# Optimization experiments

Measured on AMD Instinct MI355X. Metric: run time of the kernel, lower is better.

## Reference

```python
import jax, jax.numpy as jnp
import numpy as np


def _conv1x1(x, w, b):
    # x: [B,C,D,H,W], w: [O,C], b: [O] -> [B,O,D,H,W]
    return jnp.einsum('bcdhw,oc->bodhw', x, w) + b[None, :, None, None, None]


def setup_inputs() -> dict:
    key = jax.random.key(0)
    ks = jax.random.split(key, 8)
    C, Cr = 64, 8  # in_channels, in_channels // 8
    B, D, H, W = 2, 8, 32, 32
    s = 0.05
    return {
        'x': jax.random.normal(ks[0], (B, C, D, H, W), jnp.float32),
        'w_b': jax.random.normal(ks[1], (Cr, C), jnp.float32) * s,
        'b_b': jnp.zeros((Cr,), jnp.float32),
        'w_c': jax.random.normal(ks[2], (Cr, C), jnp.float32) * s,
        'b_c': jnp.zeros((Cr,), jnp.float32),
        'w_d': jax.random.normal(ks[3], (C, C), jnp.float32) * s,
        'b_d': jnp.zeros((C,), jnp.float32),
        'alpha': jnp.zeros((1,), jnp.float32),
    }


def reference(x, w_b, b_b, w_c, b_c, w_d, b_d, alpha):
    B, C, D, H, W = x.shape
    N = D * H * W
    feat_b = _conv1x1(x, w_b, b_b).reshape(B, -1, N).transpose(0, 2, 1)  # [B,N,Cr]
    feat_c = _conv1x1(x, w_c, b_c).reshape(B, -1, N)                      # [B,Cr,N]
    attn = jax.nn.softmax(jnp.einsum('bnk,bkm->bnm', feat_b, feat_c), axis=-1)  # [B,N,N]
    feat_d = _conv1x1(x, w_d, b_d).reshape(B, -1, N)                      # [B,C,N]
    # feat_d @ attn^T  -> [B,C,N]
    feat_e = jnp.einsum('bcn,bmn->bcm', feat_d, attn).reshape(B, C, D, H, W)
    return alpha[0] * feat_e + x
```

## Files before the change

kernel.cpp:

```cpp
#include <hip/hip_runtime.h>


#define NB   2
#define CH   64
#define CR   8
#define NPOS 8192
#define QB   64

typedef __attribute__((ext_vector_type(8)))  __bf16 bf16x8;
typedef __attribute__((ext_vector_type(16))) float  f32x16;

__device__ inline unsigned pk_bf(float lo, float hi) {
    unsigned r;
    asm("v_cvt_pk_bf16_f32 %0, %1, %2" : "=v"(r) : "v"(lo), "v"(hi));
    return r;
}
__device__ inline unsigned short f2bf(float v) {
    return (unsigned short)(pk_bf(v, 0.f) & 0xFFFFu);
}
union U4B { uint4 u; bf16x8 b; };
__device__ inline bf16x8 as_bf(uint4 u) { U4B x; x.u = u; return x.b; }

__global__ __launch_bounds__(128) void proj_kernel(
    const float* __restrict__ x,
    const float* __restrict__ w_b, const float* __restrict__ b_b,
    const float* __restrict__ w_c,
    const float* __restrict__ w_d,
    unsigned short* __restrict__ Qb, unsigned short* __restrict__ Kb,
    unsigned short* __restrict__ VFb)
{
    __shared__ unsigned short wt[96 * 64];
    const int tid = threadIdx.x;
    const float L2E = 1.4426950408889634f;
    for (int j = tid; j < 4096; j += 128) wt[j] = f2bf(w_d[j]);
    for (int j = tid; j < 512; j += 128) {
        wt[64 * 64 + j] = f2bf(w_b[j] * L2E);
        wt[72 * 64 + j] = f2bf(w_c[j]);
    }
    __syncthreads();

    const int w  = tid >> 6, l = tid & 63, li = l & 31, h = l >> 5;
    const int ng = blockIdx.x * 64 + w * 32;
    const int b  = ng >> 13;
    const int n  = ng & (NPOS - 1);

    const f32x16 z16 = {0,0,0,0,0,0,0,0,0,0,0,0,0,0,0,0};

    uint4 af[3][4];
    #pragma unroll
    for (int t = 0; t < 3; ++t)
        #pragma unroll
        for (int ks = 0; ks < 4; ++ks)
            af[t][ks] = *(const uint4*)&wt[(t * 32 + li) * 64 + ks * 16 + 8 * h];

    f32x16 acc0 = z16, acc1 = z16, acc2 = z16;
    #pragma unroll
    for (int ks = 0; ks < 4; ++ks) {
        float xr[8];
        #pragma unroll
        for (int j = 0; j < 8; ++j)
            xr[j] = x[(size_t)(b * CH + ks * 16 + 8 * h + j) * NPOS + n + li];
        uint4 bf = make_uint4(pk_bf(xr[0], xr[1]), pk_bf(xr[2], xr[3]),
                              pk_bf(xr[4], xr[5]), pk_bf(xr[6], xr[7]));
        acc0 = __builtin_amdgcn_mfma_f32_32x32x16_bf16(as_bf(af[0][ks]), as_bf(bf), acc0, 0, 0, 0);
        acc1 = __builtin_amdgcn_mfma_f32_32x32x16_bf16(as_bf(af[1][ks]), as_bf(bf), acc1, 0, 0, 0);
        acc2 = __builtin_amdgcn_mfma_f32_32x32x16_bf16(as_bf(af[2][ks]), as_bf(bf), acc2, 0, 0, 0);
    }

    {
        const int kb = n >> 5;
        const int ks = ((li >> 4) << 1) | ((li >> 3) & 1);
        unsigned short* vf = VFb + (size_t)b * NPOS * CH
                           + (size_t)kb * 2048 + ks * 512 + (li & 7);
        #pragma unroll
        for (int r = 0; r < 16; ++r) {
            int crow = (r & 3) + 8 * (r >> 2) + 4 * h;
            vf[crow * 8]        = f2bf(acc0[r]);
            vf[(32 + crow) * 8] = f2bf(acc1[r]);
        }
    }

    {
        float bb0 = b_b[4 * h + 0] * L2E, bb1 = b_b[4 * h + 1] * L2E;
        float bb2 = b_b[4 * h + 2] * L2E, bb3 = b_b[4 * h + 3] * L2E;
        unsigned q0p = pk_bf(acc2[0] + bb0, acc2[1] + bb1);
        unsigned q1p = pk_bf(acc2[2] + bb2, acc2[3] + bb3);
        unsigned k0p = pk_bf(acc2[4], acc2[5]);
        unsigned k1p = pk_bf(acc2[6], acc2[7]);
        unsigned qa0 = q0p, qb0 = q0p, qa1 = q1p, qb1 = q1p;
        asm("v_permlane32_swap_b32 %0, %1" : "+v"(qa0), "+v"(qb0));
        asm("v_permlane32_swap_b32 %0, %1" : "+v"(qa1), "+v"(qb1));
        unsigned ka0 = k0p, kb0 = k0p, ka1 = k1p, kb1 = k1p;
        asm("v_permlane32_swap_b32 %0, %1" : "+v"(ka0), "+v"(kb0));
        asm("v_permlane32_swap_b32 %0, %1" : "+v"(ka1), "+v"(kb1));
        if (h == 0) {
            *(uint4*)(Qb + (size_t)(b * NPOS + n + li) * CR) = make_uint4(qa0, qa1, qb0, qb1);
            *(uint4*)(Kb + (size_t)(b * NPOS + n + li) * CR) = make_uint4(ka0, ka1, kb0, kb1);
        }
    }
}

__global__ __launch_bounds__(1024, 4) void attn_kernel(
    const unsigned short* __restrict__ Qb, const unsigned short* __restrict__ Kb,
    const unsigned short* __restrict__ VFb, const float* __restrict__ x,
    const float* __restrict__ alpha, const float* __restrict__ b_d,
    float* __restrict__ out)
{
    __shared__ float mbuf[4 * 2080];

    const int tid = threadIdx.x;
    const int w   = tid >> 6;
    const int l   = tid & 63;
    const int li  = l & 31;
    const int h   = l >> 5;
    const int qh  = w & 1;
    const int kh  = w >> 1;
    const int blk = (blockIdx.x & 7) * 32 + (blockIdx.x >> 3);
    const int b   = blk >> 7;
    const int q0  = (blk & 127) * QB;
    const int m   = q0 + 32 * qh + li;

    const f32x16 z16 = {0,0,0,0,0,0,0,0,0,0,0,0,0,0,0,0};
    const uint4 zero4 = make_uint4(0, 0, 0, 0);

    uint4 qf = zero4;
    if (h == 0) qf = *(const uint4*)(Qb + ((size_t)b * NPOS + m) * CR);

    f32x16 acc0 = z16, acc1 = z16;
    float dn0 = 0.f, dn1 = 0.f, dn2 = 0.f, dn3 = 0.f;

    const unsigned short* kbp = Kb + ((size_t)b * NPOS + kh * 1024 + li) * CR;
    const unsigned short* vfb = VFb + (size_t)b * NPOS * CH
                              + (size_t)kh * 32 * 2048 + h * 512 + li * 8;

#define LOADS(CC, KF, A00, A01, A10, A11) {                        \
    const unsigned short* vp_ = vfb + (size_t)(CC) * 2048;         \
    A00 = *(const uint4*)(vp_);                                    \
    A01 = *(const uint4*)(vp_ + 1024);                             \
    A10 = *(const uint4*)(vp_ + 256);                              \
    A11 = *(const uint4*)(vp_ + 1280);                             \
    if (h == 0) KF = *(const uint4*)(kbp + (size_t)(CC) * 32 * CR); }

#define COMPUTE(KF, A00, A01, A10, A11) {                                                     \
    f32x16 sv = __builtin_amdgcn_mfma_f32_32x32x16_bf16(as_bf(KF), as_bf(qf), z16, 0, 0, 0);  \
    float p0_, p1_;                                                                           \
    unsigned pa0, pa1, pb0, pb1, pc0, pc1, pd0, pd1;                                          \
    p0_ = __builtin_amdgcn_exp2f(sv[0]);  p1_ = __builtin_amdgcn_exp2f(sv[1]);                \
    dn0 += p0_ + p1_;  pa0 = pk_bf(p0_, p1_);                                                 \
    p0_ = __builtin_amdgcn_exp2f(sv[2]);  p1_ = __builtin_amdgcn_exp2f(sv[3]);                \
    dn1 += p0_ + p1_;  pa1 = pk_bf(p0_, p1_);                                                 \
    p0_ = __builtin_amdgcn_exp2f(sv[4]);  p1_ = __builtin_amdgcn_exp2f(sv[5]);                \
    dn2 += p0_ + p1_;  pb0 = pk_bf(p0_, p1_);                                                 \
    p0_ = __builtin_amdgcn_exp2f(sv[6]);  p1_ = __builtin_amdgcn_exp2f(sv[7]);                \
    dn3 += p0_ + p1_;  pb1 = pk_bf(p0_, p1_);                                                 \
    p0_ = __builtin_amdgcn_exp2f(sv[8]);  p1_ = __builtin_amdgcn_exp2f(sv[9]);                \
    dn0 += p0_ + p1_;  pc0 = pk_bf(p0_, p1_);                                                 \
    p0_ = __builtin_amdgcn_exp2f(sv[10]); p1_ = __builtin_amdgcn_exp2f(sv[11]);               \
    dn1 += p0_ + p1_;  pc1 = pk_bf(p0_, p1_);                                                 \
    p0_ = __builtin_amdgcn_exp2f(sv[12]); p1_ = __builtin_amdgcn_exp2f(sv[13]);               \
    dn2 += p0_ + p1_;  pd0 = pk_bf(p0_, p1_);                                                 \
    p0_ = __builtin_amdgcn_exp2f(sv[14]); p1_ = __builtin_amdgcn_exp2f(sv[15]);               \
    dn3 += p0_ + p1_;  pd1 = pk_bf(p0_, p1_);                                                 \
    asm("v_permlane32_swap_b32 %0, %1" : "+v"(pa0), "+v"(pb0));                               \
    asm("v_permlane32_swap_b32 %0, %1" : "+v"(pa1), "+v"(pb1));                               \
    asm("v_permlane32_swap_b32 %0, %1" : "+v"(pc0), "+v"(pd0));                               \
    asm("v_permlane32_swap_b32 %0, %1" : "+v"(pc1), "+v"(pd1));                               \
    uint4 BA = make_uint4(pa0, pa1, pb0, pb1);                                                \
    uint4 BB = make_uint4(pc0, pc1, pd0, pd1);                                                \
    acc0 = __builtin_amdgcn_mfma_f32_32x32x16_bf16(as_bf(A00), as_bf(BA), acc0, 0, 0, 0);     \
    acc0 = __builtin_amdgcn_mfma_f32_32x32x16_bf16(as_bf(A01), as_bf(BB), acc0, 0, 0, 0);     \
    acc1 = __builtin_amdgcn_mfma_f32_32x32x16_bf16(as_bf(A10), as_bf(BA), acc1, 0, 0, 0);     \
    acc1 = __builtin_amdgcn_mfma_f32_32x32x16_bf16(as_bf(A11), as_bf(BB), acc1, 0, 0, 0); }

    uint4 kfA = zero4, a00A, a01A, a10A, a11A;
    uint4 kfB = zero4, a00B, a01B, a10B, a11B;
    LOADS(0, kfA, a00A, a01A, a10A, a11A);

    for (int cc = 0; cc < 32; cc += 2) {
        LOADS(cc + 1, kfB, a00B, a01B, a10B, a11B);
        COMPUTE(kfA, a00A, a01A, a10A, a11A);
        if (cc + 2 < 32) LOADS(cc + 2, kfA, a00A, a01A, a10A, a11A);
        COMPUTE(kfB, a00B, a01B, a10B, a11B);
    }
#undef LOADS
#undef COMPUTE

    float den = (dn0 + dn1) + (dn2 + dn3);
    den += __shfl_xor(den, 32);

    for (int g = 0; g < 2; ++g) {
        for (int step = 4; step >= 1; step >>= 1) {
            if (qh == g && kh >= step && kh < 2 * step) {
                float* rg = mbuf + (kh - step) * 2080;
                #pragma unroll
                for (int r = 0; r < 16; ++r) {
                    rg[r * 64 + l]        = acc0[r];
                    rg[1024 + r * 64 + l] = acc1[r];
                }
                if (h == 0) rg[2048 + li] = den;
            }
            __syncthreads();
            if (qh == g && kh < step) {
                const float* rg = mbuf + kh * 2080;
                #pragma unroll
                for (int r = 0; r < 16; ++r) {
                    acc0[r] += rg[r * 64 + l];
                    acc1[r] += rg[1024 + r * 64 + l];
                }
                if (h == 0) den += rg[2048 + li];
            }
            __syncthreads();
        }
    }
    if (kh == 0) {
        float* rg = mbuf + qh * 2080;
        #pragma unroll
        for (int r = 0; r < 16; ++r) {
            rg[r * 64 + l]        = acc0[r];
            rg[1024 + r * 64 + l] = acc1[r];
        }
        if (h == 0) rg[2048 + li] = den;
    }
    __syncthreads();

    {
        const int c   = tid >> 4;
        const int q4  = (tid & 15) * 4;
        const int qhe = q4 >> 5, qlo = q4 & 31;
        const int tile = c >> 5, c5 = c & 31;
        const int hh  = (c5 >> 2) & 1;
        const int r   = (c5 & 3) | ((c5 >> 3) << 2);
        const float* rg = mbuf + qhe * 2080;
        float4 a   = *(const float4*)&rg[tile * 1024 + r * 64 + 32 * hh + qlo];
        float4 dnv = *(const float4*)&rg[2048 + qlo];
        float  al  = alpha[0];
        float  albd = al * b_d[c];
        size_t xo  = ((size_t)(b * CH + c)) * NPOS + q0 + q4;
        float4 xv  = *(const float4*)&x[xo];
        float4 o;
        o.x = a.x * (al / dnv.x) + albd + xv.x;
        o.y = a.y * (al / dnv.y) + albd + xv.y;
        o.z = a.z * (al / dnv.z) + albd + xv.z;
        o.w = a.w * (al / dnv.w) + albd + xv.w;
        *(float4*)&out[xo] = o;
    }
}

extern "C" void kernel_launch(void* const* d_in, const int* in_sizes, int n_in,
                              void* d_out, int out_size, void* d_ws, size_t ws_size,
                              hipStream_t stream) {
    const float* x     = (const float*)d_in[0];
    const float* w_b   = (const float*)d_in[1];
    const float* b_b   = (const float*)d_in[2];
    const float* w_c   = (const float*)d_in[3];
    const float* w_d   = (const float*)d_in[5];
    const float* b_d   = (const float*)d_in[6];
    const float* alpha = (const float*)d_in[7];
    float* out = (float*)d_out;

    unsigned short* Qw  = (unsigned short*)d_ws;
    unsigned short* Kw  = Qw + (size_t)NB * NPOS * CR;
    unsigned short* VFw = Kw + (size_t)NB * NPOS * CR;

    proj_kernel<<<256, 128, 0, stream>>>(x, w_b, b_b, w_c, w_d, Qw, Kw, VFw);
    attn_kernel<<<NB * NPOS / QB, 1024, 0, stream>>>(Qw, Kw, VFw, x, alpha, b_d, out);
}
```

Before: 44.84 us.

## Split keys across blocks, stage V in LDS, merge partials in separate kernel

```diff
diff --git a/kernel.cpp b/kernel.cpp
--- a/kernel.cpp
+++ b/kernel.cpp
@@ -5,7 +5,6 @@
 #define CH   64
 #define CR   8
 #define NPOS 8192
-#define QB   64
 
 typedef __attribute__((ext_vector_type(8)))  __bf16 bf16x8;
 typedef __attribute__((ext_vector_type(16))) float  f32x16;
@@ -17,6 +16,9 @@
 }
 __device__ inline unsigned short f2bf(float v) {
     return (unsigned short)(pk_bf(v, 0.f) & 0xFFFFu);
+}
+__device__ inline float bf2f(unsigned short s) {
+    union { unsigned u; float f; } x; x.u = (unsigned)s << 16; return x.f;
 }
 union U4B { uint4 u; bf16x8 b; };
 __device__ inline bf16x8 as_bf(uint4 u) { U4B x; x.u = u; return x.b; }
@@ -102,23 +104,21 @@
 
 __global__ __launch_bounds__(1024, 4) void attn_kernel(
     const unsigned short* __restrict__ Qb, const unsigned short* __restrict__ Kb,
-    const unsigned short* __restrict__ VFb, const float* __restrict__ x,
-    const float* __restrict__ alpha, const float* __restrict__ b_d,
-    float* __restrict__ out)
+    const unsigned short* __restrict__ VFb,
+    unsigned short* __restrict__ PO, float* __restrict__ PD)
 {
-    __shared__ float mbuf[4 * 2080];
+    __shared__ unsigned short sV[32768];
 
     const int tid = threadIdx.x;
     const int w   = tid >> 6;
     const int l   = tid & 63;
     const int li  = l & 31;
     const int h   = l >> 5;
-    const int qh  = w & 1;
-    const int kh  = w >> 1;
-    const int blk = (blockIdx.x & 7) * 32 + (blockIdx.x >> 3);
+    const int blk = blockIdx.x;
+    const int kg  = blk & 7;
+    const int qr  = (blk >> 3) & 15;
     const int b   = blk >> 7;
-    const int q0  = (blk & 127) * QB;
-    const int m   = q0 + 32 * qh + li;
+    const int m   = qr * 512 + w * 32 + li;
 
     const f32x16 z16 = {0,0,0,0,0,0,0,0,0,0,0,0,0,0,0,0};
     const uint4 zero4 = make_uint4(0, 0, 0, 0);
@@ -129,20 +129,26 @@
     f32x16 acc0 = z16, acc1 = z16;
     float dn0 = 0.f, dn1 = 0.f, dn2 = 0.f, dn3 = 0.f;
 
-    const unsigned short* kbp = Kb + ((size_t)b * NPOS + kh * 1024 + li) * CR;
-    const unsigned short* vfb = VFb + (size_t)b * NPOS * CH
-                              + (size_t)kh * 32 * 2048 + h * 512 + li * 8;
-
-#define LOADS(CC, KF, A00, A01, A10, A11) {                        \
-    const unsigned short* vp_ = vfb + (size_t)(CC) * 2048;         \
-    A00 = *(const uint4*)(vp_);                                    \
-    A01 = *(const uint4*)(vp_ + 1024);                             \
-    A10 = *(const uint4*)(vp_ + 256);                              \
-    A11 = *(const uint4*)(vp_ + 1280);                             \
-    if (h == 0) KF = *(const uint4*)(kbp + (size_t)(CC) * 32 * CR); }
-
-#define COMPUTE(KF, A00, A01, A10, A11) {                                                     \
+    const unsigned short* kq = Kb + ((size_t)b * NPOS + kg * 1024 + li) * CR;
+
+    const unsigned short* vsrc = VFb + (size_t)b * NPOS * CH + (size_t)kg * 32 * 2048;
+
+#define STAGE(HS) {                                                              \
+    const unsigned short* s_ = vsrc + (size_t)(HS) * 16384;                      \
+    const int bb_ = ((HS) & 1) * 32768 + w * 1024;                               \
+    _Pragma("unroll")                                                            \
+    for (int r_ = 0; r_ < 2; ++r_)                                               \
+        __builtin_amdgcn_global_load_lds(                                        \
+            (const __attribute__((address_space(1))) void*)(s_ + (size_t)(r_ * 1024 + w * 64 + l) * 8), \
+            (__attribute__((address_space(3))) void*)((char*)(void*)sV + bb_ + r_ * 16384), \
+            16, 0, 0); }
+
+#define CHUNKC(KF, VOFF) {                                                                    \
     f32x16 sv = __builtin_amdgcn_mfma_f32_32x32x16_bf16(as_bf(KF), as_bf(qf), z16, 0, 0, 0);  \
+    uint4 a00 = *(const uint4*)(vbh + (VOFF));                                                \
+    uint4 a01 = *(const uint4*)(vbh + (VOFF) + 2048);                                         \
+    uint4 a10 = *(const uint4*)(vbh + (VOFF) + 512);                                          \
+    uint4 a11 = *(const uint4*)(vbh + (VOFF) + 2560);                                         \
     float p0_, p1_;                                                                           \
     unsigned pa0, pa1, pb0, pb1, pc0, pc1, pd0, pd1;                                          \
     p0_ = __builtin_amdgcn_exp2f(sv[0]);  p1_ = __builtin_amdgcn_exp2f(sv[1]);                \
@@ -167,83 +173,79 @@
     asm("v_permlane32_swap_b32 %0, %1" : "+v"(pc1), "+v"(pd1));                               \
     uint4 BA = make_uint4(pa0, pa1, pb0, pb1);                                                \
     uint4 BB = make_uint4(pc0, pc1, pd0, pd1);                                                \
-    acc0 = __builtin_amdgcn_mfma_f32_32x32x16_bf16(as_bf(A00), as_bf(BA), acc0, 0, 0, 0);     \
-    acc0 = __builtin_amdgcn_mfma_f32_32x32x16_bf16(as_bf(A01), as_bf(BB), acc0, 0, 0, 0);     \
-    acc1 = __builtin_amdgcn_mfma_f32_32x32x16_bf16(as_bf(A10), as_bf(BA), acc1, 0, 0, 0);     \
-    acc1 = __builtin_amdgcn_mfma_f32_32x32x16_bf16(as_bf(A11), as_bf(BB), acc1, 0, 0, 0); }
-
-    uint4 kfA = zero4, a00A, a01A, a10A, a11A;
-    uint4 kfB = zero4, a00B, a01B, a10B, a11B;
-    LOADS(0, kfA, a00A, a01A, a10A, a11A);
-
-    for (int cc = 0; cc < 32; cc += 2) {
-        LOADS(cc + 1, kfB, a00B, a01B, a10B, a11B);
-        COMPUTE(kfA, a00A, a01A, a10A, a11A);
-        if (cc + 2 < 32) LOADS(cc + 2, kfA, a00A, a01A, a10A, a11A);
-        COMPUTE(kfB, a00B, a01B, a10B, a11B);
-    }
-#undef LOADS
-#undef COMPUTE
+    acc0 = __builtin_amdgcn_mfma_f32_32x32x16_bf16(as_bf(a00), as_bf(BA), acc0, 0, 0, 0);     \
+    acc0 = __builtin_amdgcn_mfma_f32_32x32x16_bf16(as_bf(a01), as_bf(BB), acc0, 0, 0, 0);     \
+    acc1 = __builtin_amdgcn_mfma_f32_32x32x16_bf16(as_bf(a10), as_bf(BA), acc1, 0, 0, 0);     \
+    acc1 = __builtin_amdgcn_mfma_f32_32x32x16_bf16(as_bf(a11), as_bf(BB), acc1, 0, 0, 0); }
+
+    STAGE(0);
+    uint4 kfA = zero4;
+    if (h == 0) kfA = *(const uint4*)kq;
+    __syncthreads();
+
+    for (int hs = 0; hs < 4; ++hs) {
+        if (hs < 3) STAGE(hs + 1);
+        const char* vbh = (const char*)(const void*)sV
+                        + (hs & 1) * 32768 + h * 1024 + li * 16;
+        const unsigned short* kq_hs = kq + hs * 8 * 256;
+        #pragma unroll
+        for (int cp = 0; cp < 8; ++cp) {
+            uint4 kfn = zero4;
+            if (h == 0 && (hs * 8 + cp) < 31)
+                kfn = *(const uint4*)(kq_hs + (cp + 1) * 256);
+            CHUNKC(kfA, cp * 4096);
+            kfA = kfn;
+        }
+        __syncthreads();
+    }
+#undef STAGE
+#undef CHUNKC
 
     float den = (dn0 + dn1) + (dn2 + dn3);
     den += __shfl_xor(den, 32);
 
-    for (int g = 0; g < 2; ++g) {
-        for (int step = 4; step >= 1; step >>= 1) {
-            if (qh == g && kh >= step && kh < 2 * step) {
-                float* rg = mbuf + (kh - step) * 2080;
-                #pragma unroll
-                for (int r = 0; r < 16; ++r) {
-                    rg[r * 64 + l]        = acc0[r];
-                    rg[1024 + r * 64 + l] = acc1[r];
-                }
-                if (h == 0) rg[2048 + li] = den;
-            }
-            __syncthreads();
-            if (qh == g && kh < step) {
-                const float* rg = mbuf + kh * 2080;
-                #pragma unroll
-                for (int r = 0; r < 16; ++r) {
-                    acc0[r] += rg[r * 64 + l];
-                    acc1[r] += rg[1024 + r * 64 + l];
-                }
-                if (h == 0) den += rg[2048 + li];
-            }
-            __syncthreads();
-        }
-    }
-    if (kh == 0) {
-        float* rg = mbuf + qh * 2080;
+    {
+        const int g = kg * 2 + b;
         #pragma unroll
         for (int r = 0; r < 16; ++r) {
-            rg[r * 64 + l]        = acc0[r];
-            rg[1024 + r * 64 + l] = acc1[r];
-        }
-        if (h == 0) rg[2048 + li] = den;
-    }
-    __syncthreads();
-
-    {
-        const int c   = tid >> 4;
-        const int q4  = (tid & 15) * 4;
-        const int qhe = q4 >> 5, qlo = q4 & 31;
-        const int tile = c >> 5, c5 = c & 31;
-        const int hh  = (c5 >> 2) & 1;
-        const int r   = (c5 & 3) | ((c5 >> 3) << 2);
-        const float* rg = mbuf + qhe * 2080;
-        float4 a   = *(const float4*)&rg[tile * 1024 + r * 64 + 32 * hh + qlo];
-        float4 dnv = *(const float4*)&rg[2048 + qlo];
-        float  al  = alpha[0];
-        float  albd = al * b_d[c];
-        size_t xo  = ((size_t)(b * CH + c)) * NPOS + q0 + q4;
-        float4 xv  = *(const float4*)&x[xo];
-        float4 o;
-        o.x = a.x * (al / dnv.x) + albd + xv.x;
-        o.y = a.y * (al / dnv.y) + albd + xv.y;
-        o.z = a.z * (al / dnv.z) + albd + xv.z;
-        o.w = a.w * (al / dnv.w) + albd + xv.w;
-        *(float4*)&out[xo] = o;
-    }
+            int crow = (r & 3) + 8 * (r >> 2) + 4 * h;
+            PO[((size_t)g * 64 + crow) * NPOS + m]      = f2bf(acc0[r]);
+            PO[((size_t)g * 64 + 32 + crow) * NPOS + m] = f2bf(acc1[r]);
+        }
+        if (h == 0) PD[(size_t)g * NPOS + m] = den;
+    }
+}
+
+__global__ __launch_bounds__(256) void merge_kernel(
+    const unsigned short* __restrict__ PO, const float* __restrict__ PD,
+    const float* __restrict__ x, const float* __restrict__ alpha,
+    const float* __restrict__ b_d, float* __restrict__ out)
+{
+    const int t  = blockIdx.x * 256 + threadIdx.x;
+    const int q4 = (t & 2047) * 4;
+    const int bc = t >> 11;
+    const int b  = bc >> 6, c = bc & 63;
+
+    float4 o = make_float4(0.f, 0.f, 0.f, 0.f);
+    float4 d = make_float4(0.f, 0.f, 0.f, 0.f);
+    #pragma unroll
+    for (int kg = 0; kg < 8; ++kg) {
+        const int g = kg * 2 + b;
+        ushort4 u = *(const ushort4*)(PO + ((size_t)g * 64 + c) * NPOS + q4);
+        o.x += bf2f(u.x); o.y += bf2f(u.y); o.z += bf2f(u.z); o.w += bf2f(u.w);
+        float4 dv = *(const float4*)(PD + (size_t)g * NPOS + q4);
+        d.x += dv.x; d.y += dv.y; d.z += dv.z; d.w += dv.w;
+    }
+    const float al = alpha[0];
+    const float albd = al * b_d[c];
+    const size_t xo = ((size_t)bc << 13) + q4;
+    float4 xv = *(const float4*)&x[xo];
+    float4 r;
+    r.x = o.x * (al / d.x) + albd + xv.x;
+    r.y = o.y * (al / d.y) + albd + xv.y;
+    r.z = o.z * (al / d.z) + albd + xv.z;
+    r.w = o.w * (al / d.w) + albd + xv.w;
+    *(float4*)&out[xo] = r;
 }
 
 extern "C" void kernel_launch(void* const* d_in, const int* in_sizes, int n_in,
@@ -261,7 +263,10 @@
     unsigned short* Qw  = (unsigned short*)d_ws;
     unsigned short* Kw  = Qw + (size_t)NB * NPOS * CR;
     unsigned short* VFw = Kw + (size_t)NB * NPOS * CR;
+    unsigned short* PO  = VFw + (size_t)NB * NPOS * CH;
+    float*          PD  = (float*)(PO + (size_t)16 * CH * NPOS);
 
     proj_kernel<<<256, 128, 0, stream>>>(x, w_b, b_b, w_c, w_d, Qw, Kw, VFw);
-    attn_kernel<<<NB * NPOS / QB, 1024, 0, stream>>>(Qw, Kw, VFw, x, alpha, b_d, out);
-}
+    attn_kernel<<<256, 1024, 0, stream>>>(Qw, Kw, VFw, PO, PD);
+    merge_kernel<<<1024, 256, 0, stream>>>(PO, PD, x, alpha, b_d, out);
+}
```

After: 110.5 us. +146.3%, slower.
